# Kernel optimization log

Hardware: AMD Instinct MI355X
Metric: run time of the kernel (lower is better)

Reference implementation:

```python
import jax, jax.numpy as jnp
import numpy as np

EMB, HEADS = 1024, 16
HD = EMB // HEADS


def setup_inputs() -> dict:
    key = jax.random.key(0)
    ks = jax.random.split(key, 9)
    B, T, C = 4, 2048, EMB
    s = 1.0 / np.sqrt(C)
    return {
        "x": jax.random.normal(ks[0], (B, T, C), jnp.float32),
        "Wq": jax.random.normal(ks[1], (C, C), jnp.float32) * s,
        "bq": jnp.zeros((C,), jnp.float32),
        "Wk": jax.random.normal(ks[2], (C, C), jnp.float32) * s,
        "bk": jnp.zeros((C,), jnp.float32),
        "Wv": jax.random.normal(ks[3], (C, C), jnp.float32) * s,
        "bv": jnp.zeros((C,), jnp.float32),
        "Wo": jax.random.normal(ks[4], (C, C), jnp.float32) * s,
        "bo": jnp.zeros((C,), jnp.float32),
    }


def _attn(x, Wq, bq, Wk, bk, Wv, bv, Wo, bo):
    B, T, C = x.shape
    # [B,T,C] -> [B,H,T,hd]
    def split(h):
        return h.reshape(B, T, HEADS, HD).transpose(0, 2, 1, 3)
    q = split(x @ Wq + bq)
    k = split(x @ Wk + bk)
    v = split(x @ Wv + bv)
    att = jnp.einsum("bhtd,bhsd->bhts", q, k) * (1.0 / np.sqrt(HD))
    causal = jnp.tril(jnp.ones((T, T), bool))  # [T,T]
    att = jnp.where(causal, att, -jnp.inf)
    att = jax.nn.softmax(att, axis=-1)
    y = jnp.einsum("bhts,bhsd->bhtd", att, v)
    y = y.transpose(0, 2, 1, 3).reshape(B, T, C)
    return y @ Wo + bo


def reference(x, Wq, bq, Wk, bk, Wv, bv, Wo, bo):
    return _attn(x, Wq, bq, Wk, bk, Wv, bv, Wo, bo)
```

## Files before the change

### kernel.cpp

```cpp
#include <hip/hip_runtime.h>
#include <cmath>

#define EMB 1024
#define HEADS 16
#define HD 64
#define BATCH 4
#define SEQ 2048
#define MTOT (BATCH * SEQ)

typedef __attribute__((ext_vector_type(8))) short short8;
typedef __attribute__((ext_vector_type(4))) float f32x4;
typedef __attribute__((ext_vector_type(16))) float f32x16;

__device__ __forceinline__ float b2f(unsigned short u) {
  union { unsigned int i; float f; } c; c.i = ((unsigned int)u) << 16; return c.f;
}
__device__ __forceinline__ unsigned short f2b(float f) {
  union { float f; unsigned int i; } c; c.f = f;
  unsigned int x = c.i;
  return (unsigned short)((x + 0x7fffu + ((x >> 16) & 1u)) >> 16);
}

#define GLD16(gp, lp) __builtin_amdgcn_global_load_lds( \
    (__attribute__((address_space(1))) unsigned int*)(gp), \
    (__attribute__((address_space(3))) unsigned int*)(lp), 16, 0, 0)

__global__ __launch_bounds__(256) void transpose_w4(
    const float* __restrict__ W0, const float* __restrict__ W1,
    const float* __restrict__ W2, const float* __restrict__ W3,
    unsigned short* __restrict__ Wt) {
  __shared__ float T[32][33];
  const int z = blockIdx.z;
  const float* W = (z == 0) ? W0 : (z == 1) ? W1 : (z == 2) ? W2 : W3;
  unsigned short* out = Wt + (size_t)z * EMB * EMB;
  const int k0 = blockIdx.x * 32, n0 = blockIdx.y * 32;
  const int tx = threadIdx.x, ty = threadIdx.y;
#pragma unroll
  for (int r = 0; r < 4; ++r)
    T[ty + r * 8][tx] = W[(size_t)(k0 + ty + r * 8) * EMB + n0 + tx];
  __syncthreads();
#pragma unroll
  for (int r = 0; r < 4; ++r)
    out[(size_t)(n0 + ty + r * 8) * EMB + k0 + tx] = f2b(T[tx][ty + r * 8]);
}

__global__ __launch_bounds__(256) void convert_x(
    const float* __restrict__ x, unsigned short* __restrict__ xb) {
  const size_t i = ((size_t)blockIdx.x * 256 + threadIdx.x) * 8;
  const float4 a = *(const float4*)(x + i);
  const float4 b = *(const float4*)(x + i + 4);
  ushort4 lo = {f2b(a.x), f2b(a.y), f2b(a.z), f2b(a.w)};
  ushort4 hi = {f2b(b.x), f2b(b.y), f2b(b.z), f2b(b.w)};
  *(ushort4*)(xb + i) = lo;
  *(ushort4*)(xb + i + 4) = hi;
}

template <int OUTMODE>
__global__ __launch_bounds__(256) void gemm_mfma(
    const unsigned short* __restrict__ A, const unsigned short* __restrict__ Bt,
    const float* __restrict__ bias, void* __restrict__ outp) {
  __shared__ unsigned short As[128 * 32];
  __shared__ unsigned short Bs[128 * 32];
  const int tid = threadIdx.x;
  const int w = tid >> 6, lane = tid & 63;
  const int g = lane >> 4, m = lane & 15;
  const int row0 = blockIdx.x * 128, col0 = blockIdx.y * 128;
  const int wm = (w >> 1) * 64, wn = (w & 1) * 64;

  f32x4 acc[4][4];
#pragma unroll
  for (int i = 0; i < 4; ++i)
#pragma unroll
    for (int j = 0; j < 4; ++j) acc[i][j] = (f32x4){0.f, 0.f, 0.f, 0.f};

  for (int kb = 0; kb < EMB; kb += 32) {
    if (kb) __syncthreads();
#pragma unroll
    for (int i = 0; i < 2; ++i) {
      const int segb = w * 64 + i * 256;
      const int seg = segb + lane;
      GLD16(Bt + (size_t)(col0 + (seg >> 2)) * EMB + kb + (seg & 3) * 8,
            &Bs[segb * 8]);
    }
#pragma unroll
    for (int i = 0; i < 2; ++i) {
      const int segb = w * 64 + i * 256;
      const int seg = segb + lane;
      GLD16(A + (size_t)(row0 + (seg >> 2)) * EMB + kb + (seg & 3) * 8,
            &As[segb * 8]);
    }
    __syncthreads();

    short8 af[4], bf[4];
#pragma unroll
    for (int i = 0; i < 4; ++i)
      af[i] = *(const short8*)&As[(wm + i * 16 + m) * 32 + g * 8];
#pragma unroll
    for (int j = 0; j < 4; ++j)
      bf[j] = *(const short8*)&Bs[(wn + j * 16 + m) * 32 + g * 8];
#pragma unroll
    for (int i = 0; i < 4; ++i)
#pragma unroll
      for (int j = 0; j < 4; ++j)
        acc[i][j] = __builtin_amdgcn_mfma_f32_16x16x32_bf16(af[i], bf[j],
                                                            acc[i][j], 0, 0, 0);
  }

  float bv[4];
#pragma unroll
  for (int j = 0; j < 4; ++j) bv[j] = bias[col0 + wn + j * 16 + m];

#pragma unroll
  for (int i = 0; i < 4; ++i)
#pragma unroll
    for (int j = 0; j < 4; ++j)
#pragma unroll
      for (int r = 0; r < 4; ++r) {
        const size_t row = row0 + wm + i * 16 + g * 4 + r;
        const size_t col = col0 + wn + j * 16 + m;
        const float val = acc[i][j][r] + bv[j];
        if constexpr (OUTMODE == 0) ((float*)outp)[row * EMB + col] = val;
        else ((unsigned short*)outp)[row * EMB + col] = f2b(val);
      }
}

__global__ __launch_bounds__(256) void gemm_qkv(
    const unsigned short* __restrict__ A, const unsigned short* __restrict__ Wt,
    const float* __restrict__ b0, const float* __restrict__ b1,
    const float* __restrict__ b2, unsigned short* __restrict__ out) {
  __shared__ unsigned short As[128 * 32];
  __shared__ unsigned short Bs[128 * 32];
  const int z = blockIdx.z;
  const unsigned short* Bt = Wt + (size_t)z * EMB * EMB;
  const float* bias = (z == 0) ? b0 : ((z == 1) ? b1 : b2);
  const int tid = threadIdx.x;
  const int w = tid >> 6, lane = tid & 63;
  const int g = lane >> 4, m = lane & 15;
  const int row0 = blockIdx.x * 128, col0 = blockIdx.y * 128;
  const int wm = (w >> 1) * 64, wn = (w & 1) * 64;

  f32x4 acc[4][4];
#pragma unroll
  for (int i = 0; i < 4; ++i)
#pragma unroll
    for (int j = 0; j < 4; ++j) acc[i][j] = (f32x4){0.f, 0.f, 0.f, 0.f};

  for (int kb = 0; kb < EMB; kb += 32) {
    if (kb) __syncthreads();
#pragma unroll
    for (int i = 0; i < 2; ++i) {
      const int segb = w * 64 + i * 256;
      const int seg = segb + lane;
      GLD16(Bt + (size_t)(col0 + (seg >> 2)) * EMB + kb + (seg & 3) * 8,
            &Bs[segb * 8]);
    }
#pragma unroll
    for (int i = 0; i < 2; ++i) {
      const int segb = w * 64 + i * 256;
      const int seg = segb + lane;
      GLD16(A + (size_t)(row0 + (seg >> 2)) * EMB + kb + (seg & 3) * 8,
            &As[segb * 8]);
    }
    __syncthreads();

    short8 af[4], bf[4];
#pragma unroll
    for (int i = 0; i < 4; ++i)
      af[i] = *(const short8*)&As[(wm + i * 16 + m) * 32 + g * 8];
#pragma unroll
    for (int j = 0; j < 4; ++j)
      bf[j] = *(const short8*)&Bs[(wn + j * 16 + m) * 32 + g * 8];
#pragma unroll
    for (int i = 0; i < 4; ++i)
#pragma unroll
      for (int j = 0; j < 4; ++j)
        acc[i][j] = __builtin_amdgcn_mfma_f32_16x16x32_bf16(af[i], bf[j],
                                                            acc[i][j], 0, 0, 0);
  }

  float bv[4];
#pragma unroll
  for (int j = 0; j < 4; ++j) bv[j] = bias[col0 + wn + j * 16 + m];

  if (z == 2) {
    unsigned short* Vt = out + (size_t)2 * MTOT * EMB;
    const int bi = row0 >> 11;
    const int tb = (row0 & 2047) + wm;
#pragma unroll
    for (int i = 0; i < 4; ++i)
#pragma unroll
      for (int j = 0; j < 4; ++j) {
        const int col = col0 + wn + j * 16 + m;
        const int t0 = tb + i * 16 + g * 4;
        ushort4 pv = {f2b(acc[i][j][0] + bv[j]), f2b(acc[i][j][1] + bv[j]),
                      f2b(acc[i][j][2] + bv[j]), f2b(acc[i][j][3] + bv[j])};
        *(ushort4*)&Vt[(size_t)(bi * 1024 + col) * SEQ + t0] = pv;
      }
  } else {
    unsigned short* O = out + (size_t)z * MTOT * EMB;
#pragma unroll
    for (int i = 0; i < 4; ++i)
#pragma unroll
      for (int j = 0; j < 4; ++j)
#pragma unroll
        for (int r = 0; r < 4; ++r) {
          const size_t row = row0 + wm + i * 16 + g * 4 + r;
          const size_t col = col0 + wn + j * 16 + m;
          O[row * EMB + col] = f2b(acc[i][j][r] + bv[j]);
        }
  }
}

__global__ __launch_bounds__(256, 4) void flash_mfma(
    const unsigned short* __restrict__ Qg, const unsigned short* __restrict__ Kg,
    const unsigned short* __restrict__ Vtg, unsigned short* __restrict__ Yg) {
  __shared__ unsigned short Kl[2][64 * 64];
  __shared__ unsigned short Vl[2][64 * 64];
  const int tid = threadIdx.x;
  const int w = tid >> 6, lane = tid & 63;
  const int ql = lane & 31;
  const int hi = lane >> 5;

  const int gid = blockIdx.x;
  const int g2 = gid & 3;
  const int hb = (gid >> 2) & 63;
  const int g8 = gid >> 8;
  const int q4 = g2 * 4 + g8;
  const int qb = (q4 & 1) ? (q4 >> 1) : (15 - (q4 >> 1));
  const int bi = hb >> 4, hd = hb & 15;

  const size_t base = ((size_t)bi * SEQ) * EMB + (size_t)hd * HD;
  const size_t vtrow0 = (size_t)(bi * HEADS + hd) * HD;

  const int r8 = lane >> 3;
  const int c8 = ((lane & 7) ^ r8) * 8;

#define STAGE(tile_, buf_)                                                  \
  do {                                                                      \
    const int s0_ = (tile_) * 64;                                           \
    _Pragma("unroll")                                                       \
    for (int L = 0; L < 2; ++L) {                                           \
      const int rb_ = 16 * w + 8 * L;                                       \
      GLD16(Kg + base + (size_t)(s0_ + rb_ + r8) * EMB + c8,                \
            &Kl[buf_][rb_ * 64]);                                           \
    }                                                                       \
    _Pragma("unroll")                                                       \
    for (int L = 0; L < 2; ++L) {                                           \
      const int rb_ = 16 * w + 8 * L;                                       \
      GLD16(Vtg + (vtrow0 + rb_ + r8) * SEQ + s0_ + c8,                     \
            &Vl[buf_][rb_ * 64]);                                           \
    }                                                                       \
  } while (0)

  const int q0w = qb * 128 + 32 * w;
  const int q = q0w + ql;

  short8 qf[4];
#pragma unroll
  for (int s = 0; s < 4; ++s) {
    const uint4 u = *(const uint4*)(
        Qg + base + (size_t)q * EMB + s * 16 + hi * 8);
    const unsigned short* t = (const unsigned short*)&u;
    short8 qv;
#pragma unroll
    for (int j = 0; j < 8; ++j) qv[j] = (short)f2b(b2f(t[j]) * 0.18033688f);
    qf[s] = qv;
  }

  f32x16 acc[2];
#pragma unroll
  for (int db = 0; db < 2; ++db)
#pragma unroll
    for (int i = 0; i < 16; ++i) acc[db][i] = 0.f;
  float m_r = -INFINITY, l_r = 0.f;

  const int nt = 2 * qb + 2;
  STAGE(0, 0);

  int buf = 0;
  for (int t = 0; t < nt; ++t) {
    asm volatile("s_waitcnt vmcnt(0)" ::: "memory");
    __builtin_amdgcn_s_barrier();
    if (t + 1 < nt) STAGE(t + 1, buf ^ 1);
    const int s0 = t * 64;
    if (s0 <= q0w + 31) {
      const unsigned short* K0 = Kl[buf];
      const unsigned short* V0 = Vl[buf];

      f32x16 sA[2];
      __builtin_amdgcn_s_setprio(1);
#pragma unroll
      for (int n = 0; n < 2; ++n) {
        const int row = 32 * n + ql;
        const int rb = row * 64, rk = row & 7;
        f32x16 z;
#pragma unroll
        for (int i = 0; i < 16; ++i) z[i] = 0.f;
#pragma unroll
        for (int s = 0; s < 4; ++s) {
          const short8 kf =
              *(const short8*)&K0[rb + (((2 * s + hi) ^ rk) * 8)];
          z = __builtin_amdgcn_mfma_f32_32x32x16_bf16(kf, qf[s], z, 0, 0, 0);
        }
        sA[n] = z;
      }
      __builtin_amdgcn_s_setprio(0);

      if (s0 + 63 > q) {
#pragma unroll
        for (int n = 0; n < 2; ++n)
#pragma unroll
          for (int r = 0; r < 16; ++r)
            if (s0 + 32 * n + (r & 3) + 8 * (r >> 2) + 4 * hi > q)
              sA[n][r] = -INFINITY;
      }

      float tmax = -INFINITY;
#pragma unroll
      for (int n = 0; n < 2; ++n)
#pragma unroll
        for (int r = 0; r < 16; ++r) tmax = fmaxf(tmax, sA[n][r]);
      tmax = fmaxf(tmax, __shfl_xor(tmax, 32));

      if (!__all(tmax - m_r <= 11.f)) {
        const float nm = fmaxf(m_r, tmax);
        float sc;
        const float d0 = m_r - nm;
        asm("v_exp_f32 %0, %1" : "=v"(sc) : "v"(d0));
#pragma unroll
        for (int db = 0; db < 2; ++db)
#pragma unroll
          for (int i = 0; i < 16; ++i) acc[db][i] *= sc;
        l_r *= sc;
        m_r = nm;
      }

      float ps = 0.f;
#pragma unroll
      for (int n = 0; n < 2; ++n)
#pragma unroll
        for (int r = 0; r < 16; ++r) {
          float p;
          const float d1 = sA[n][r] - m_r;
          asm("v_exp_f32 %0, %1" : "=v"(p) : "v"(d1));
          sA[n][r] = p;
          ps += p;
        }
      ps += __shfl_xor(ps, 32);
      l_r += ps;

      unsigned int pk[2][8];
#pragma unroll
      for (int n = 0; n < 2; ++n)
#pragma unroll
        for (int i = 0; i < 8; ++i) {
          unsigned int d;
          asm("v_cvt_pk_bf16_f32 %0, %1, %2"
              : "=v"(d) : "v"(sA[n][2 * i]), "v"(sA[n][2 * i + 1]));
          pk[n][i] = d;
        }
      union { unsigned int u[4]; short8 s; } pf[4];
#pragma unroll
      for (int ks = 0; ks < 4; ++ks) {
        const int n = ks >> 1, k4 = (ks & 1) * 4;
        unsigned int a0 = pk[n][k4 + 0], a1 = pk[n][k4 + 1];
        unsigned int b0 = pk[n][k4 + 2], b1 = pk[n][k4 + 3];
        asm("v_permlane32_swap_b32 %0, %1" : "+v"(a0), "+v"(b0));
        asm("v_permlane32_swap_b32 %0, %1" : "+v"(a1), "+v"(b1));
        pf[ks].u[0] = a0; pf[ks].u[1] = a1;
        pf[ks].u[2] = b0; pf[ks].u[3] = b1;
      }

      __builtin_amdgcn_s_setprio(1);
#pragma unroll
      for (int db = 0; db < 2; ++db) {
        const int row = 32 * db + ql;
        const int rb = row * 64, rk = row & 7;
#pragma unroll
        for (int ks = 0; ks < 4; ++ks) {
          const short8 vf =
              *(const short8*)&V0[rb + (((2 * ks + hi) ^ rk) * 8)];
          acc[db] = __builtin_amdgcn_mfma_f32_32x32x16_bf16(vf, pf[ks].s,
                                                            acc[db], 0, 0, 0);
        }
      }
      __builtin_amdgcn_s_setprio(0);
    }
    buf ^= 1;
  }

  const float iv = 1.f / l_r;
  unsigned short* Yrow = Yg + base + (size_t)q * EMB;
#pragma unroll
  for (int db = 0; db < 2; ++db)
#pragma unroll
    for (int r = 0; r < 16; r += 2) {
      unsigned int d;
      const float lo = acc[db][r] * iv, hh = acc[db][r + 1] * iv;
      asm("v_cvt_pk_bf16_f32 %0, %1, %2" : "=v"(d) : "v"(lo), "v"(hh));
      const int col = 32 * db + (r & 3) + 8 * (r >> 2) + 4 * hi;
      *(unsigned int*)(Yrow + col) = d;
    }
#undef STAGE
}

extern "C" void kernel_launch(void* const* d_in, const int* in_sizes, int n_in,
                              void* d_out, int out_size, void* d_ws, size_t ws_size,
                              hipStream_t stream) {
  const float* x  = (const float*)d_in[0];
  const float* Wq = (const float*)d_in[1];
  const float* bq = (const float*)d_in[2];
  const float* Wk = (const float*)d_in[3];
  const float* bk = (const float*)d_in[4];
  const float* Wv = (const float*)d_in[5];
  const float* bv = (const float*)d_in[6];
  const float* Wo = (const float*)d_in[7];
  const float* bo = (const float*)d_in[8];
  float* out = (float*)d_out;

  unsigned short* wqt = (unsigned short*)d_ws;
  unsigned short* wot = wqt + (size_t)3 * EMB * EMB;
  unsigned short* Q  = wqt + (size_t)4 * EMB * EMB;
  unsigned short* K  = Q + (size_t)MTOT * EMB;
  unsigned short* Vt = K + (size_t)MTOT * EMB;
  unsigned short* Y  = Vt + (size_t)MTOT * EMB;
  unsigned short* xb = Y + (size_t)MTOT * EMB;

  transpose_w4<<<dim3(EMB / 32, EMB / 32, 4), dim3(32, 8), 0, stream>>>(
      Wq, Wk, Wv, Wo, wqt);
  convert_x<<<dim3(MTOT * EMB / (256 * 8)), 256, 0, stream>>>(x, xb);

  gemm_qkv<<<dim3(MTOT / 128, EMB / 128, 3), 256, 0, stream>>>(
      xb, wqt, bq, bk, bv, Q);
  flash_mfma<<<dim3(1024), 256, 0, stream>>>(Q, K, Vt, Y);
  gemm_mfma<0><<<dim3(MTOT / 128, EMB / 128), 256, 0, stream>>>(
      Y, wot, bo, out);
}
```

Baseline: 163.1 us.

## Double-buffer GEMM LDS tiles and XOR-swizzle chunks to avoid bank conflicts

Both the QKV projection GEMM and the output GEMM now keep two LDS buffers per operand. The next K-slice is prefetched with global_load_lds while MFMAs run on the current one, and each iteration needs one wait plus barrier instead of two syncthreads. The 16-byte chunk position within each 32-element row is XOR-swizzled by row to cut LDS bank conflicts on the fragment reads. LDS use per block doubles, which may reduce occupancy. The single barrier relies on the vmcnt wait ordering being correct against reuse of the buffer being overwritten.

```diff
diff --git a/kernel.cpp b/kernel.cpp
--- a/kernel.cpp
+++ b/kernel.cpp
@@ -55,12 +55,52 @@
   *(ushort4*)(xb + i + 4) = hi;
 }
 
+#define GEMM_STAGE(Asrc_, Bsrc_, kb_, b_)                                   \
+  do {                                                                      \
+    _Pragma("unroll")                                                       \
+    for (int i_ = 0; i_ < 2; ++i_) {                                        \
+      const int segb_ = w * 64 + i_ * 256;                                  \
+      const int seg_ = segb_ + lane;                                        \
+      const int r_ = seg_ >> 2, c_ = seg_ & 3;                              \
+      const int sc_ = (c_ ^ (r_ & 3)) * 8;                                  \
+      GLD16((Bsrc_) + (size_t)(col0 + r_) * EMB + (kb_) + sc_,              \
+            &Bs[b_][segb_ * 8]);                                            \
+      GLD16((Asrc_) + (size_t)(row0 + r_) * EMB + (kb_) + sc_,              \
+            &As[b_][segb_ * 8]);                                            \
+    }                                                                       \
+  } while (0)
+
+#define GEMM_KLOOP(Asrc_, Bsrc_)                                            \
+  GEMM_STAGE(Asrc_, Bsrc_, 0, 0);                                           \
+  int buf = 0;                                                              \
+  for (int kb = 0; kb < EMB; kb += 32) {                                    \
+    asm volatile("s_waitcnt vmcnt(0)" ::: "memory");                        \
+    __builtin_amdgcn_s_barrier();                                           \
+    if (kb + 32 < EMB) GEMM_STAGE(Asrc_, Bsrc_, kb + 32, buf ^ 1);          \
+    short8 af[4], bf[4];                                                    \
+    _Pragma("unroll")                                                       \
+    for (int i = 0; i < 4; ++i)                                             \
+      af[i] = *(const short8*)                                              \
+          &As[buf][(wm + i * 16 + m) * 32 + ((g ^ (m & 3)) * 8)];           \
+    _Pragma("unroll")                                                       \
+    for (int j = 0; j < 4; ++j)                                             \
+      bf[j] = *(const short8*)                                              \
+          &Bs[buf][(wn + j * 16 + m) * 32 + ((g ^ (m & 3)) * 8)];           \
+    _Pragma("unroll")                                                       \
+    for (int i = 0; i < 4; ++i)                                             \
+      _Pragma("unroll")                                                     \
+      for (int j = 0; j < 4; ++j)                                           \
+        acc[i][j] = __builtin_amdgcn_mfma_f32_16x16x32_bf16(                \
+            af[i], bf[j], acc[i][j], 0, 0, 0);                              \
+    buf ^= 1;                                                               \
+  }
+
 template <int OUTMODE>
 __global__ __launch_bounds__(256) void gemm_mfma(
     const unsigned short* __restrict__ A, const unsigned short* __restrict__ Bt,
     const float* __restrict__ bias, void* __restrict__ outp) {
-  __shared__ unsigned short As[128 * 32];
-  __shared__ unsigned short Bs[128 * 32];
+  __shared__ unsigned short As[2][128 * 32];
+  __shared__ unsigned short Bs[2][128 * 32];
   const int tid = threadIdx.x;
   const int w = tid >> 6, lane = tid & 63;
   const int g = lane >> 4, m = lane & 15;
@@ -73,38 +113,7 @@
 #pragma unroll
     for (int j = 0; j < 4; ++j) acc[i][j] = (f32x4){0.f, 0.f, 0.f, 0.f};
 
-  for (int kb = 0; kb < EMB; kb += 32) {
-    if (kb) __syncthreads();
-#pragma unroll
-    for (int i = 0; i < 2; ++i) {
-      const int segb = w * 64 + i * 256;
-      const int seg = segb + lane;
-      GLD16(Bt + (size_t)(col0 + (seg >> 2)) * EMB + kb + (seg & 3) * 8,
-            &Bs[segb * 8]);
-    }
-#pragma unroll
-    for (int i = 0; i < 2; ++i) {
-      const int segb = w * 64 + i * 256;
-      const int seg = segb + lane;
-      GLD16(A + (size_t)(row0 + (seg >> 2)) * EMB + kb + (seg & 3) * 8,
-            &As[segb * 8]);
-    }
-    __syncthreads();
-
-    short8 af[4], bf[4];
-#pragma unroll
-    for (int i = 0; i < 4; ++i)
-      af[i] = *(const short8*)&As[(wm + i * 16 + m) * 32 + g * 8];
-#pragma unroll
-    for (int j = 0; j < 4; ++j)
-      bf[j] = *(const short8*)&Bs[(wn + j * 16 + m) * 32 + g * 8];
-#pragma unroll
-    for (int i = 0; i < 4; ++i)
-#pragma unroll
-      for (int j = 0; j < 4; ++j)
-        acc[i][j] = __builtin_amdgcn_mfma_f32_16x16x32_bf16(af[i], bf[j],
-                                                            acc[i][j], 0, 0, 0);
-  }
+  GEMM_KLOOP(A, Bt)
 
   float bv[4];
 #pragma unroll
@@ -128,8 +137,8 @@
     const unsigned short* __restrict__ A, const unsigned short* __restrict__ Wt,
     const float* __restrict__ b0, const float* __restrict__ b1,
     const float* __restrict__ b2, unsigned short* __restrict__ out) {
-  __shared__ unsigned short As[128 * 32];
-  __shared__ unsigned short Bs[128 * 32];
+  __shared__ unsigned short As[2][128 * 32];
+  __shared__ unsigned short Bs[2][128 * 32];
   const int z = blockIdx.z;
   const unsigned short* Bt = Wt + (size_t)z * EMB * EMB;
   const float* bias = (z == 0) ? b0 : ((z == 1) ? b1 : b2);
@@ -145,38 +154,7 @@
 #pragma unroll
     for (int j = 0; j < 4; ++j) acc[i][j] = (f32x4){0.f, 0.f, 0.f, 0.f};
 
-  for (int kb = 0; kb < EMB; kb += 32) {
-    if (kb) __syncthreads();
-#pragma unroll
-    for (int i = 0; i < 2; ++i) {
-      const int segb = w * 64 + i * 256;
-      const int seg = segb + lane;
-      GLD16(Bt + (size_t)(col0 + (seg >> 2)) * EMB + kb + (seg & 3) * 8,
-            &Bs[segb * 8]);
-    }
-#pragma unroll
-    for (int i = 0; i < 2; ++i) {
-      const int segb = w * 64 + i * 256;
-      const int seg = segb + lane;
-      GLD16(A + (size_t)(row0 + (seg >> 2)) * EMB + kb + (seg & 3) * 8,
-            &As[segb * 8]);
-    }
-    __syncthreads();
-
-    short8 af[4], bf[4];
-#pragma unroll
-    for (int i = 0; i < 4; ++i)
-      af[i] = *(const short8*)&As[(wm + i * 16 + m) * 32 + g * 8];
-#pragma unroll
-    for (int j = 0; j < 4; ++j)
-      bf[j] = *(const short8*)&Bs[(wn + j * 16 + m) * 32 + g * 8];
-#pragma unroll
-    for (int i = 0; i < 4; ++i)
-#pragma unroll
-      for (int j = 0; j < 4; ++j)
-        acc[i][j] = __builtin_amdgcn_mfma_f32_16x16x32_bf16(af[i], bf[j],
-                                                            acc[i][j], 0, 0, 0);
-  }
+  GEMM_KLOOP(A, Bt)
 
   float bv[4];
 #pragma unroll
```

After: 181.7 us. 1.11x slower.
